# Optimization experiments

Measured on AMD Instinct MI355X. Metric: run time of the kernel, lower is better.

Reference implementation:

```python
import jax, jax.numpy as jnp
import numpy as np

def setup_inputs() -> dict:
    key = jax.random.key(0)
    input_tensor = jax.random.normal(key, (32, 2048, 1024), dtype=jnp.float32)
    return {"input_tensor": input_tensor}

def reference(input_tensor):
    # (x + 2) * 3 - 4, then elementwise relu (the torch loop is just per-scalar relu)
    return jax.nn.relu((input_tensor + 2.0) * 3.0 - 4.0)
```

## Files before the change

kernel.cpp:

```cpp
#include <hip/hip_runtime.h>
#include <hip/hip_bf16.h>


__global__ void __launch_bounds__(256) fused_affine_relu_kernel(
    const float4* __restrict__ in, float4* __restrict__ out, int n4) {
    int idx = blockIdx.x * blockDim.x + threadIdx.x;
    int stride = gridDim.x * blockDim.x;
    for (int i = idx; i < n4; i += stride) {
        float4 v = in[i];
        float4 r;
        r.x = fmaxf((v.x + 2.0f) * 3.0f - 4.0f, 0.0f);
        r.y = fmaxf((v.y + 2.0f) * 3.0f - 4.0f, 0.0f);
        r.z = fmaxf((v.z + 2.0f) * 3.0f - 4.0f, 0.0f);
        r.w = fmaxf((v.w + 2.0f) * 3.0f - 4.0f, 0.0f);
        out[i] = r;
    }
}

extern "C" void kernel_launch(void* const* d_in, const int* in_sizes, int n_in,
                              void* d_out, int out_size, void* d_ws, size_t ws_size,
                              hipStream_t stream) {
    const float* in = (const float*)d_in[0];
    float* out = (float*)d_out;
    int n = in_sizes[0];
    int n4 = n / 4;

    const int block = 256;
    int blocks = (n4 + block - 1) / block;
    if (blocks > 2048) blocks = 2048;

    fused_affine_relu_kernel<<<blocks, block, 0, stream>>>(
        (const float4*)in, (float4*)out, n4);
}
```

Measured before the change: 107.1 us.

## Replace grid-stride loop with unrolled nontemporal x4 kernel and tail kernel

Swaps the capped grid-stride loop for a non-looping kernel in which each thread issues four independent 16-byte nontemporal loads and stores, launching one block per 4096 elements, plus a scalar tail kernel for leftovers. The affine is folded algebraically into a single fma (x*3+2). The aim is more memory-level parallelism and less cache pollution for a purely bandwidth-bound streaming op. The cost is a much larger grid and slightly different float rounding from the folded fma.

```diff
diff --git a/kernel.cpp b/kernel.cpp
--- a/kernel.cpp
+++ b/kernel.cpp
@@ -2,19 +2,34 @@
 #include <hip/hip_bf16.h>
 
 
-__global__ void __launch_bounds__(256) fused_affine_relu_kernel(
-    const float4* __restrict__ in, float4* __restrict__ out, int n4) {
-    int idx = blockIdx.x * blockDim.x + threadIdx.x;
-    int stride = gridDim.x * blockDim.x;
-    for (int i = idx; i < n4; i += stride) {
-        float4 v = in[i];
-        float4 r;
-        r.x = fmaxf((v.x + 2.0f) * 3.0f - 4.0f, 0.0f);
-        r.y = fmaxf((v.y + 2.0f) * 3.0f - 4.0f, 0.0f);
-        r.z = fmaxf((v.z + 2.0f) * 3.0f - 4.0f, 0.0f);
-        r.w = fmaxf((v.w + 2.0f) * 3.0f - 4.0f, 0.0f);
-        out[i] = r;
-    }
+typedef float f32x4 __attribute__((ext_vector_type(4)));
+
+__device__ __forceinline__ f32x4 affine_relu(f32x4 v) {
+    f32x4 r;
+    r.x = fmaxf(fmaf(v.x, 3.0f, 2.0f), 0.0f);
+    r.y = fmaxf(fmaf(v.y, 3.0f, 2.0f), 0.0f);
+    r.z = fmaxf(fmaf(v.z, 3.0f, 2.0f), 0.0f);
+    r.w = fmaxf(fmaf(v.w, 3.0f, 2.0f), 0.0f);
+    return r;
+}
+
+__global__ void __launch_bounds__(256) fused_affine_relu_x4(
+    const f32x4* __restrict__ in, f32x4* __restrict__ out) {
+    int i = blockIdx.x * 1024 + threadIdx.x;
+    f32x4 v0 = __builtin_nontemporal_load(in + i);
+    f32x4 v1 = __builtin_nontemporal_load(in + i + 256);
+    f32x4 v2 = __builtin_nontemporal_load(in + i + 512);
+    f32x4 v3 = __builtin_nontemporal_load(in + i + 768);
+    __builtin_nontemporal_store(affine_relu(v0), out + i);
+    __builtin_nontemporal_store(affine_relu(v1), out + i + 256);
+    __builtin_nontemporal_store(affine_relu(v2), out + i + 512);
+    __builtin_nontemporal_store(affine_relu(v3), out + i + 768);
+}
+
+__global__ void __launch_bounds__(256) fused_affine_relu_tail(
+    const float* __restrict__ in, float* __restrict__ out, int start, int n) {
+    int i = start + blockIdx.x * blockDim.x + threadIdx.x;
+    if (i < n) out[i] = fmaxf(fmaf(in[i], 3.0f, 2.0f), 0.0f);
 }
 
 extern "C" void kernel_launch(void* const* d_in, const int* in_sizes, int n_in,
@@ -23,12 +38,17 @@
     const float* in = (const float*)d_in[0];
     float* out = (float*)d_out;
     int n = in_sizes[0];
-    int n4 = n / 4;
 
-    const int block = 256;
-    int blocks = (n4 + block - 1) / block;
-    if (blocks > 2048) blocks = 2048;
-
-    fused_affine_relu_kernel<<<blocks, block, 0, stream>>>(
-        (const float4*)in, (float4*)out, n4);
+    const int elems_per_block = 256 * 16;
+    int main_blocks = n / elems_per_block;
+    if (main_blocks > 0) {
+        fused_affine_relu_x4<<<main_blocks, 256, 0, stream>>>(
+            (const f32x4*)in, (f32x4*)out);
+    }
+    int done = main_blocks * elems_per_block;
+    int rem = n - done;
+    if (rem > 0) {
+        int tb = (rem + 255) / 256;
+        fused_affine_relu_tail<<<tb, 256, 0, stream>>>(in, out, done, n);
+    }
 }
```

After: 87.60 us. 18.2% less time.
